# Kernel tuning notes

Measured on AMD Instinct MI355X. Metric: run time of the kernel, lower is better.

## Reference

```python
import jax, jax.numpy as jnp
import numpy as np

IN_F, OUT_F, BATCH = 4096, 11008, 8

def setup_inputs() -> dict:
    key = jax.random.key(0)
    k_x, k_s, k_sg, k_b = jax.random.split(key, 4)
    x = jax.random.normal(k_x, (BATCH, IN_F), dtype=jnp.float32)
    # stored codes in [1, 255] as in QINSCodec.encode (uint8 storage)
    stored = jax.random.randint(k_s, (OUT_F, IN_F), 1, 256, dtype=jnp.int32).astype(jnp.uint8)
    # sign in {-1, +1} (int8 storage)
    sign = (jax.random.randint(k_sg, (OUT_F, IN_F), 0, 2, dtype=jnp.int32) * 2 - 1).astype(jnp.int8)
    log_min = jnp.array([-10.0], dtype=jnp.float32)
    log_max = jnp.array([0.0], dtype=jnp.float32)
    bias = jax.random.normal(k_b, (OUT_F,), dtype=jnp.float32) * 0.02
    return {"x": x, "stored": stored, "sign": sign, "log_min": log_min, "log_max": log_max, "bias": bias}

def _decode(stored, sign, log_min, log_max):
    # QINSCodec.decode: normalized = (255 - stored)/254; w = sign * exp(log_min + normalized*(log_max-log_min))
    normalized = (255.0 - stored.astype(jnp.float32)) / 254.0
    log_w = log_min + normalized * (log_max - log_min)
    return sign.astype(jnp.float32) * jnp.exp(log_w)

def reference(x, stored, sign, log_min, log_max, bias):
    lmin = log_min[0]
    lmax = log_max[0]
    w = _decode(stored, sign, lmin, lmax)            # [OUT_F, IN_F]
    return x @ w.T + bias                            # F.linear(x, w, bias)
```

## Files before the change

### kernel.cpp

```cpp
#include <hip/hip_runtime.h>
#include <stdint.h>

#define IN_F   4096
#define OUT_F  11008
#define BATCH  8
#define WAVES  4
#define RPW    2
#define RPB    (WAVES*RPW)
#define CHUNK  128
#define NCHUNK (IN_F/CHUNK)
#define NSLOT  4
#define SLOTI  (3*RPB*CHUNK)

typedef __attribute__((address_space(1))) const uint32_t* gas_t;
typedef __attribute__((address_space(3))) uint32_t* las_t;

#define DMA16(gsrc, ldst) \
    __builtin_amdgcn_global_load_lds((gas_t)(gsrc), (las_t)(ldst), 16, 0, 0)

#define SBAR() __builtin_amdgcn_sched_barrier(0)
#define VWAIT(N)                                                             \
    do {                                                                     \
        asm volatile("s_waitcnt vmcnt(" #N ")" ::: "memory");                \
        SBAR();                                                              \
    } while (0)

__device__ __forceinline__ float qins_decode(int code, int sgn, float d0, float d1) {
    const float e = __builtin_amdgcn_exp2f(fmaf((float)code, d1, d0));
    const uint32_t m = ((uint32_t)sgn) & 0x80000000u;
    return __uint_as_float(__float_as_uint(e) ^ m);
}

__global__ __launch_bounds__(256, 3)
void qins_linear_kernel(const float* __restrict__ x,
                        const uint32_t* __restrict__ stored,
                        const uint32_t* __restrict__ sign,
                        const float* __restrict__ log_min,
                        const float* __restrict__ log_max,
                        const float* __restrict__ bias,
                        float* __restrict__ out)
{
    __shared__ int lds[NSLOT][SLOTI];

    const int tid  = threadIdx.x;
    const int lane = tid & 63;
    const int wave = tid >> 6;
    const int o0   = blockIdx.x * RPB;

    const float lmin = log_min[0];
    const float lmax = log_max[0];
    const float L2E  = 1.44269504088896340736f;
    const float d1 = -(lmax - lmin) * (L2E / 254.0f);
    const float d0 = (lmin + (lmax - lmin) * (255.0f / 254.0f)) * L2E;

    const int sub = lane >> 5;
    const int i32 = (lane & 31) * 4;
    const uint32_t* gs = stored + (size_t)(o0 + 2 * wave + sub) * IN_F + i32;
    const uint32_t* gg = sign   + (size_t)(o0 + 2 * wave + sub) * IN_F + i32;
    const uint32_t* gx = (const uint32_t*)x + (size_t)(2 * wave + sub) * IN_F + i32;

#define ISSUE(T, K)                                                          \
    do {                                                                     \
        const int _ip = (K) * CHUNK;                                         \
        DMA16(gs + _ip, &lds[T][wave * 256]);                                \
        DMA16(gg + _ip, &lds[T][1024 + wave * 256]);                         \
        DMA16(gx + _ip, &lds[T][2048 + wave * 256]);                         \
    } while (0)

    float acc[RPW][BATCH];
#pragma unroll
    for (int r = 0; r < RPW; ++r)
#pragma unroll
        for (int b = 0; b < BATCH; ++b) acc[r][b] = 0.0f;

    ISSUE(0, 0);
    ISSUE(1, 1);
    ISSUE(2, 2);
    SBAR();

#pragma unroll 1
    for (int k = 0; k < NCHUNK; ++k) {
        if (k < NCHUNK - 2)       VWAIT(6);
        else if (k == NCHUNK - 2) VWAIT(3);
        else                      VWAIT(0);
        __builtin_amdgcn_s_barrier();
        SBAR();

        if (k + 3 < NCHUNK)
            ISSUE((k + 3) & (NSLOT - 1), k + 3);
        SBAR();

        {
            const int cur = k & (NSLOT - 1);
            const int li  = lane * 2;
            const int2 c0 = *reinterpret_cast<const int2*>(&lds[cur][wave * 256 + li]);
            const int2 c1 = *reinterpret_cast<const int2*>(&lds[cur][wave * 256 + 128 + li]);
            const int2 g0 = *reinterpret_cast<const int2*>(&lds[cur][1024 + wave * 256 + li]);
            const int2 g1 = *reinterpret_cast<const int2*>(&lds[cur][1024 + wave * 256 + 128 + li]);
            const float w00 = qins_decode(c0.x, g0.x, d0, d1);
            const float w01 = qins_decode(c0.y, g0.y, d0, d1);
            const float w10 = qins_decode(c1.x, g1.x, d0, d1);
            const float w11 = qins_decode(c1.y, g1.y, d0, d1);
#pragma unroll
            for (int b = 0; b < BATCH; ++b) {
                const float2 xv = *reinterpret_cast<const float2*>(
                    &lds[cur][2048 + (b >> 1) * 256 + (b & 1) * 128 + li]);
                acc[0][b] = fmaf(w01, xv.y, fmaf(w00, xv.x, acc[0][b]));
                acc[1][b] = fmaf(w11, xv.y, fmaf(w10, xv.x, acc[1][b]));
            }
        }
    }

#pragma unroll
    for (int r = 0; r < RPW; ++r)
#pragma unroll
        for (int b = 0; b < BATCH; ++b) {
            float v = acc[r][b];
#pragma unroll
            for (int s = 32; s >= 1; s >>= 1)
                v += __shfl_xor(v, s, 64);
            acc[r][b] = v;
        }

    if (lane == 0) {
#pragma unroll
        for (int r = 0; r < RPW; ++r) {
            const int row = o0 + 2 * wave + r;
            const float bv = bias[row];
#pragma unroll
            for (int b = 0; b < BATCH; ++b)
                out[(size_t)b * OUT_F + row] = acc[r][b] + bv;
        }
    }
#undef ISSUE
}

extern "C" void kernel_launch(void* const* d_in, const int* in_sizes, int n_in,
                              void* d_out, int out_size, void* d_ws, size_t ws_size,
                              hipStream_t stream)
{
    const float*    x      = (const float*)d_in[0];
    const uint32_t* stored = (const uint32_t*)d_in[1];
    const uint32_t* sign   = (const uint32_t*)d_in[2];
    const float*    lmin   = (const float*)d_in[3];
    const float*    lmax   = (const float*)d_in[4];
    const float*    bias   = (const float*)d_in[5];
    float* out = (float*)d_out;

    dim3 grid(OUT_F / RPB), block(WAVES * 64);
    qins_linear_kernel<<<grid, block, 0, stream>>>(x, stored, sign, lmin, lmax, bias, out);
}
```

Before: 78.64 us.

## Halve chunk size with 4-byte LDS DMA and raise occupancy to 4 blocks

Shrinks the per-iteration K chunk from 128 to 64 and switches the global-to-LDS DMA from 16-byte to 4-byte per lane, issuing six loads per chunk instead of three. The smaller LDS footprint allows launch bounds of 4 blocks per CU instead of 3, meant to raise occupancy and memory parallelism in this bandwidth-bound GEMV. The cost is twice as many loop iterations and barriers, and narrower per-lane transfers that may lower DMA efficiency.

```diff
diff --git a/kernel.cpp b/kernel.cpp
--- a/kernel.cpp
+++ b/kernel.cpp
@@ -7,7 +7,7 @@
 #define WAVES  4
 #define RPW    2
 #define RPB    (WAVES*RPW)
-#define CHUNK  128
+#define CHUNK  64
 #define NCHUNK (IN_F/CHUNK)
 #define NSLOT  4
 #define SLOTI  (3*RPB*CHUNK)
@@ -15,8 +15,8 @@
 typedef __attribute__((address_space(1))) const uint32_t* gas_t;
 typedef __attribute__((address_space(3))) uint32_t* las_t;
 
-#define DMA16(gsrc, ldst) \
-    __builtin_amdgcn_global_load_lds((gas_t)(gsrc), (las_t)(ldst), 16, 0, 0)
+#define DMA4(gsrc, ldst) \
+    __builtin_amdgcn_global_load_lds((gas_t)(gsrc), (las_t)(ldst), 4, 0, 0)
 
 #define SBAR() __builtin_amdgcn_sched_barrier(0)
 #define VWAIT(N)                                                             \
@@ -31,7 +31,7 @@
     return __uint_as_float(__float_as_uint(e) ^ m);
 }
 
-__global__ __launch_bounds__(256, 3)
+__global__ __launch_bounds__(256, 4)
 void qins_linear_kernel(const float* __restrict__ x,
                         const uint32_t* __restrict__ stored,
                         const uint32_t* __restrict__ sign,
@@ -46,6 +46,7 @@
     const int lane = tid & 63;
     const int wave = tid >> 6;
     const int o0   = blockIdx.x * RPB;
+    const int w128 = wave * 128;
 
     const float lmin = log_min[0];
     const float lmax = log_max[0];
@@ -53,18 +54,22 @@
     const float d1 = -(lmax - lmin) * (L2E / 254.0f);
     const float d0 = (lmin + (lmax - lmin) * (255.0f / 254.0f)) * L2E;
 
-    const int sub = lane >> 5;
-    const int i32 = (lane & 31) * 4;
-    const uint32_t* gs = stored + (size_t)(o0 + 2 * wave + sub) * IN_F + i32;
-    const uint32_t* gg = sign   + (size_t)(o0 + 2 * wave + sub) * IN_F + i32;
-    const uint32_t* gx = (const uint32_t*)x + (size_t)(2 * wave + sub) * IN_F + i32;
+    const uint32_t* gs0 = stored + (size_t)(o0 + 2 * wave)     * IN_F + lane;
+    const uint32_t* gs1 = stored + (size_t)(o0 + 2 * wave + 1) * IN_F + lane;
+    const uint32_t* gg0 = sign   + (size_t)(o0 + 2 * wave)     * IN_F + lane;
+    const uint32_t* gg1 = sign   + (size_t)(o0 + 2 * wave + 1) * IN_F + lane;
+    const uint32_t* gx0 = (const uint32_t*)x + (size_t)(2 * wave)     * IN_F + lane;
+    const uint32_t* gx1 = (const uint32_t*)x + (size_t)(2 * wave + 1) * IN_F + lane;
 
 #define ISSUE(T, K)                                                          \
     do {                                                                     \
         const int _ip = (K) * CHUNK;                                         \
-        DMA16(gs + _ip, &lds[T][wave * 256]);                                \
-        DMA16(gg + _ip, &lds[T][1024 + wave * 256]);                         \
-        DMA16(gx + _ip, &lds[T][2048 + wave * 256]);                         \
+        DMA4(gs0 + _ip, &lds[T][w128]);                                      \
+        DMA4(gs1 + _ip, &lds[T][w128 + 64]);                                 \
+        DMA4(gg0 + _ip, &lds[T][512 + w128]);                                \
+        DMA4(gg1 + _ip, &lds[T][512 + w128 + 64]);                           \
+        DMA4(gx0 + _ip, &lds[T][1024 + w128]);                               \
+        DMA4(gx1 + _ip, &lds[T][1024 + w128 + 64]);                          \
     } while (0)
 
     float acc[RPW][BATCH];
@@ -80,8 +85,8 @@
 
 #pragma unroll 1
     for (int k = 0; k < NCHUNK; ++k) {
-        if (k < NCHUNK - 2)       VWAIT(6);
-        else if (k == NCHUNK - 2) VWAIT(3);
+        if (k <= NCHUNK - 3)      VWAIT(12);
+        else if (k == NCHUNK - 2) VWAIT(6);
         else                      VWAIT(0);
         __builtin_amdgcn_s_barrier();
         SBAR();
@@ -92,21 +97,18 @@
 
         {
             const int cur = k & (NSLOT - 1);
-            const int li  = lane * 2;
-            const int2 c0 = *reinterpret_cast<const int2*>(&lds[cur][wave * 256 + li]);
-            const int2 c1 = *reinterpret_cast<const int2*>(&lds[cur][wave * 256 + 128 + li]);
-            const int2 g0 = *reinterpret_cast<const int2*>(&lds[cur][1024 + wave * 256 + li]);
-            const int2 g1 = *reinterpret_cast<const int2*>(&lds[cur][1024 + wave * 256 + 128 + li]);
-            const float w00 = qins_decode(c0.x, g0.x, d0, d1);
-            const float w01 = qins_decode(c0.y, g0.y, d0, d1);
-            const float w10 = qins_decode(c1.x, g1.x, d0, d1);
-            const float w11 = qins_decode(c1.y, g1.y, d0, d1);
+            const int c0 = lds[cur][w128 + lane];
+            const int c1 = lds[cur][w128 + 64 + lane];
+            const int g0 = lds[cur][512 + w128 + lane];
+            const int g1 = lds[cur][512 + w128 + 64 + lane];
+            const float w0 = qins_decode(c0, g0, d0, d1);
+            const float w1 = qins_decode(c1, g1, d0, d1);
 #pragma unroll
             for (int b = 0; b < BATCH; ++b) {
-                const float2 xv = *reinterpret_cast<const float2*>(
-                    &lds[cur][2048 + (b >> 1) * 256 + (b & 1) * 128 + li]);
-                acc[0][b] = fmaf(w01, xv.y, fmaf(w00, xv.x, acc[0][b]));
-                acc[1][b] = fmaf(w11, xv.y, fmaf(w10, xv.x, acc[1][b]));
+                const float xv = __int_as_float(
+                    lds[cur][1024 + (b >> 1) * 128 + (b & 1) * 64 + lane]);
+                acc[0][b] = fmaf(w0, xv, acc[0][b]);
+                acc[1][b] = fmaf(w1, xv, acc[1][b]);
             }
         }
     }
```

Measured after the change: 78.17 us. No clear change (-0.6%).

## Replace global-to-LDS DMA ring with register-staged double-buffered LDS pipeline

Applied to the files above, without the earlier changes.

Global loads of codes, signs and x now go into registers and are written to LDS with inline ds_write_b128, replacing the 4-slot direct global_load_lds ring with a 2-slot double buffer. The loop is unrolled by two and alternates register sets A/B, so the next chunk's global load overlaps the current chunk's compute. LDS reads use inline ds_read_b64 with immediate offsets and an explicit lgkmcnt wait. Launch bounds drop from 3 to 2 blocks per CU, which frees registers but lowers occupancy and leaves less prefetch depth in flight.

```diff
diff --git a/kernel.cpp b/kernel.cpp
--- a/kernel.cpp
+++ b/kernel.cpp
@@ -9,21 +9,21 @@
 #define RPB    (WAVES*RPW)
 #define CHUNK  128
 #define NCHUNK (IN_F/CHUNK)
-#define NSLOT  4
 #define SLOTI  (3*RPB*CHUNK)
+#define SLOTB  (SLOTI*4)
 
-typedef __attribute__((address_space(1))) const uint32_t* gas_t;
 typedef __attribute__((address_space(3))) uint32_t* las_t;
-
-#define DMA16(gsrc, ldst) \
-    __builtin_amdgcn_global_load_lds((gas_t)(gsrc), (las_t)(ldst), 16, 0, 0)
+typedef int i32x2 __attribute__((ext_vector_type(2)));
+typedef int i32x4 __attribute__((ext_vector_type(4)));
 
 #define SBAR() __builtin_amdgcn_sched_barrier(0)
-#define VWAIT(N)                                                             \
-    do {                                                                     \
-        asm volatile("s_waitcnt vmcnt(" #N ")" ::: "memory");                \
-        SBAR();                                                              \
-    } while (0)
+#define LGKM0() asm volatile("s_waitcnt lgkmcnt(0)" ::: "memory")
+
+#define DSREAD(dst, addr, OFF)                                               \
+    asm volatile("ds_read_b64 %0, %1 offset:" #OFF : "=v"(dst) : "v"(addr))
+#define DSWRITE(addr, data, OFF)                                             \
+    asm volatile("ds_write_b128 %0, %1 offset:" #OFF                         \
+                 :: "v"(addr), "v"(data) : "memory")
 
 __device__ __forceinline__ float qins_decode(int code, int sgn, float d0, float d1) {
     const float e = __builtin_amdgcn_exp2f(fmaf((float)code, d1, d0));
@@ -31,16 +31,16 @@
     return __uint_as_float(__float_as_uint(e) ^ m);
 }
 
-__global__ __launch_bounds__(256, 3)
+__global__ __launch_bounds__(256, 2)
 void qins_linear_kernel(const float* __restrict__ x,
-                        const uint32_t* __restrict__ stored,
-                        const uint32_t* __restrict__ sign,
+                        const int* __restrict__ stored,
+                        const int* __restrict__ sign,
                         const float* __restrict__ log_min,
                         const float* __restrict__ log_max,
                         const float* __restrict__ bias,
                         float* __restrict__ out)
 {
-    __shared__ int lds[NSLOT][SLOTI];
+    __shared__ int lds[2][SLOTI];
 
     const int tid  = threadIdx.x;
     const int lane = tid & 63;
@@ -55,17 +55,31 @@
 
     const int sub = lane >> 5;
     const int i32 = (lane & 31) * 4;
-    const uint32_t* gs = stored + (size_t)(o0 + 2 * wave + sub) * IN_F + i32;
-    const uint32_t* gg = sign   + (size_t)(o0 + 2 * wave + sub) * IN_F + i32;
-    const uint32_t* gx = (const uint32_t*)x + (size_t)(2 * wave + sub) * IN_F + i32;
+    const int* gs = stored + (size_t)(o0 + 2 * wave + sub) * IN_F + i32;
+    const int* gg = sign   + (size_t)(o0 + 2 * wave + sub) * IN_F + i32;
+    const int* gx = (const int*)x + (size_t)(2 * wave + sub) * IN_F + i32;
 
-#define ISSUE(T, K)                                                          \
+    i32x4 As, Ag, Ax, Bs, Bg, Bx;
+#define GLOAD(P, K)                                                          \
     do {                                                                     \
         const int _ip = (K) * CHUNK;                                         \
-        DMA16(gs + _ip, &lds[T][wave * 256]);                                \
-        DMA16(gg + _ip, &lds[T][1024 + wave * 256]);                         \
-        DMA16(gx + _ip, &lds[T][2048 + wave * 256]);                         \
+        P##s = *reinterpret_cast<const i32x4*>(gs + _ip);                    \
+        P##g = *reinterpret_cast<const i32x4*>(gg + _ip);                    \
+        P##x = *reinterpret_cast<const i32x4*>(gx + _ip);                    \
     } while (0)
+
+    const uint32_t ldsb = (uint32_t)(uintptr_t)(las_t)&lds[0][0];
+    const uint32_t wrb  = ldsb + (uint32_t)(wave * 1024 + lane * 16);
+#define WRITE(P, SLOT)                                                       \
+    do {                                                                     \
+        const uint32_t _a = wrb + (SLOT) * SLOTB;                            \
+        DSWRITE(_a, P##s, 0);                                                \
+        DSWRITE(_a, P##g, 4096);                                             \
+        DSWRITE(_a, P##x, 8192);                                             \
+    } while (0)
+
+    const uint32_t baseW = ldsb + (uint32_t)(wave * 1024 + lane * 8);
+    const uint32_t baseX = ldsb + 8192u + (uint32_t)(lane * 8);
 
     float acc[RPW][BATCH];
 #pragma unroll
@@ -73,43 +87,71 @@
 #pragma unroll
         for (int b = 0; b < BATCH; ++b) acc[r][b] = 0.0f;
 
-    ISSUE(0, 0);
-    ISSUE(1, 1);
-    ISSUE(2, 2);
-    SBAR();
+#define COMPUTE(K, SLOT)                                                     \
+    do {                                                                     \
+        const uint32_t aw = baseW + (SLOT) * SLOTB;                          \
+        const uint32_t ax = baseX + (SLOT) * SLOTB;                          \
+        i32x2 c0, c1, g0, g1, xv[BATCH];                                     \
+        DSREAD(c0, aw, 0);                                                   \
+        DSREAD(c1, aw, 512);                                                 \
+        DSREAD(g0, aw, 4096);                                                \
+        DSREAD(g1, aw, 4608);                                                \
+        DSREAD(xv[0], ax, 0);                                                \
+        DSREAD(xv[1], ax, 512);                                              \
+        DSREAD(xv[2], ax, 1024);                                             \
+        DSREAD(xv[3], ax, 1536);                                             \
+        DSREAD(xv[4], ax, 2048);                                             \
+        DSREAD(xv[5], ax, 2560);                                             \
+        DSREAD(xv[6], ax, 3072);                                             \
+        DSREAD(xv[7], ax, 3584);                                             \
+        LGKM0();                                                             \
+        SBAR();                                                              \
+        const float w00 = qins_decode(c0.x, g0.x, d0, d1);                   \
+        const float w01 = qins_decode(c0.y, g0.y, d0, d1);                   \
+        const float w10 = qins_decode(c1.x, g1.x, d0, d1);                   \
+        const float w11 = qins_decode(c1.y, g1.y, d0, d1);                   \
+        _Pragma("unroll")                                                    \
+        for (int b = 0; b < BATCH; ++b) {                                    \
+            const float xlo = __int_as_float(xv[b].x);                       \
+            const float xhi = __int_as_float(xv[b].y);                       \
+            acc[0][b] = fmaf(w01, xhi, fmaf(w00, xlo, acc[0][b]));           \
+            acc[1][b] = fmaf(w11, xhi, fmaf(w10, xlo, acc[1][b]));           \
+        }                                                                    \
+    } while (0)
+
+#define BARRIER()                                                            \
+    do {                                                                     \
+        LGKM0();                                                             \
+        SBAR();                                                              \
+        __builtin_amdgcn_s_barrier();                                        \
+        SBAR();                                                              \
+    } while (0)
+
+    GLOAD(B, 0);
+    WRITE(B, 0);
+    GLOAD(A, 1);
+    BARRIER();
 
 #pragma unroll 1
-    for (int k = 0; k < NCHUNK; ++k) {
-        if (k < NCHUNK - 2)       VWAIT(6);
-        else if (k == NCHUNK - 2) VWAIT(3);
-        else                      VWAIT(0);
-        __builtin_amdgcn_s_barrier();
+    for (int k = 0; k < NCHUNK - 2; k += 2) {
+        GLOAD(B, k + 2);
         SBAR();
-
-        if (k + 3 < NCHUNK)
-            ISSUE((k + 3) & (NSLOT - 1), k + 3);
+        COMPUTE(k, 0);
         SBAR();
-
-        {
-            const int cur = k & (NSLOT - 1);
-            const int li  = lane * 2;
-            const int2 c0 = *reinterpret_cast<const int2*>(&lds[cur][wave * 256 + li]);
-            const int2 c1 = *reinterpret_cast<const int2*>(&lds[cur][wave * 256 + 128 + li]);
-            const int2 g0 = *reinterpret_cast<const int2*>(&lds[cur][1024 + wave * 256 + li]);
-            const int2 g1 = *reinterpret_cast<const int2*>(&lds[cur][1024 + wave * 256 + 128 + li]);
-            const float w00 = qins_decode(c0.x, g0.x, d0, d1);
-            const float w01 = qins_decode(c0.y, g0.y, d0, d1);
-            const float w10 = qins_decode(c1.x, g1.x, d0, d1);
-            const float w11 = qins_decode(c1.y, g1.y, d0, d1);
-#pragma unroll
-            for (int b = 0; b < BATCH; ++b) {
-                const float2 xv = *reinterpret_cast<const float2*>(
-                    &lds[cur][2048 + (b >> 1) * 256 + (b & 1) * 128 + li]);
-                acc[0][b] = fmaf(w01, xv.y, fmaf(w00, xv.x, acc[0][b]));
-                acc[1][b] = fmaf(w11, xv.y, fmaf(w10, xv.x, acc[1][b]));
-            }
-        }
+        WRITE(A, 1);
+        BARRIER();
+        if (k + 3 < NCHUNK) { GLOAD(A, k + 3); }
+        SBAR();
+        COMPUTE(k + 1, 1);
+        SBAR();
+        WRITE(B, 0);
+        BARRIER();
     }
+    COMPUTE(NCHUNK - 2, 0);
+    SBAR();
+    WRITE(A, 1);
+    BARRIER();
+    COMPUTE(NCHUNK - 1, 1);
 
 #pragma unroll
     for (int r = 0; r < RPW; ++r)
@@ -132,19 +174,18 @@
                 out[(size_t)b * OUT_F + row] = acc[r][b] + bv;
         }
     }
-#undef ISSUE
 }
 
 extern "C" void kernel_launch(void* const* d_in, const int* in_sizes, int n_in,
                               void* d_out, int out_size, void* d_ws, size_t ws_size,
                               hipStream_t stream)
 {
-    const float*    x      = (const float*)d_in[0];
-    const uint32_t* stored = (const uint32_t*)d_in[1];
-    const uint32_t* sign   = (const uint32_t*)d_in[2];
-    const float*    lmin   = (const float*)d_in[3];
-    const float*    lmax   = (const float*)d_in[4];
-    const float*    bias   = (const float*)d_in[5];
+    const float* x      = (const float*)d_in[0];
+    const int*   stored = (const int*)d_in[1];
+    const int*   sign   = (const int*)d_in[2];
+    const float* lmin   = (const float*)d_in[3];
+    const float* lmax   = (const float*)d_in[4];
+    const float* bias   = (const float*)d_in[5];
     float* out = (float*)d_out;
 
     dim3 grid(OUT_F / RPB), block(WAVES * 64);
```

Result: faster. 71.85 us (-8.6%).
